# Performance work log

Hardware: AMD Instinct MI355X
Metric: run time of the kernel (lower is better)

Reference implementation:

```python
import jax, jax.numpy as jnp
import numpy as np

N_NODES = 100000
N_EDGES = 3200000
NFEAT = 256
NHID = 256
NOUT = 128


def setup_inputs() -> dict:
    key = jax.random.key(0)
    ks = jax.random.split(key, 8)
    stdv1 = 1.0 / np.sqrt(NHID)
    stdv2 = 1.0 / np.sqrt(NOUT)
    return {
        "feat": jax.random.normal(ks[0], (N_NODES, NFEAT), dtype=jnp.float32),
        "row": jax.random.randint(ks[1], (N_EDGES,), 0, N_NODES, dtype=jnp.int32),
        "col": jax.random.randint(ks[2], (N_EDGES,), 0, N_NODES, dtype=jnp.int32),
        "edge_weight": jax.random.uniform(ks[3], (N_EDGES,), dtype=jnp.float32),
        "W1": jax.random.uniform(ks[4], (NFEAT, NHID), jnp.float32, -stdv1, stdv1),
        "b1": jax.random.uniform(ks[5], (NHID,), jnp.float32, -stdv1, stdv1),
        "W2": jax.random.uniform(ks[6], (NHID, NOUT), jnp.float32, -stdv2, stdv2),
        "b2": jax.random.uniform(ks[7], (NOUT,), jnp.float32, -stdv2, stdv2),
    }


def _spmm(row, col, edge_weight, x, n_nodes):
    # sparse.mm(adj, x): out[i] = sum_e w[e] * x[col[e]] for row[e] == i
    msgs = x[col] * edge_weight[:, None]  # [E, F] gather + scale
    return jax.ops.segment_sum(msgs, row, num_segments=n_nodes)


def reference(feat, row, col, edge_weight, W1, b1, W2, b2):
    # Layer 1: GraphConvolution + ReLU (dropout is identity in eval mode)
    h = _spmm(row, col, edge_weight, feat @ W1, feat.shape[0]) + b1
    h = jax.nn.relu(h)
    # Layer 2: GraphConvolution (no activation on final layer)
    out = _spmm(row, col, edge_weight, h @ W2, feat.shape[0]) + b2
    return out
```

## Files before the change

kernel.cpp:

```cpp
#include <hip/hip_runtime.h>
#include <hip/hip_bf16.h>

#define M_NODES 100000
#define E_EDGES 3200000
#define NBUCK 196
#define BSHIFT 9
#define BCAP 24576
#define K3_EPB 8192
#define K3_BLOCKS 391
#define TILESM 391

typedef __attribute__((ext_vector_type(8))) short short8;
typedef __attribute__((ext_vector_type(4))) float f32x4;
typedef __attribute__((ext_vector_type(2))) float f32x2;

__device__ inline unsigned short f2bf(float f) {
  __hip_bfloat16 h = __float2bfloat16(f);
  return __builtin_bit_cast(unsigned short, h);
}

#if __has_builtin(__builtin_amdgcn_cvt_pk_f32_fp8) && __has_builtin(__builtin_amdgcn_cvt_pk_fp8_f32)
#define HW_FP8 1
#endif

#ifndef HW_FP8
__device__ inline float fp8_dec1(unsigned int b) {
  const unsigned int s = (b >> 7) & 1u, e = (b >> 3) & 15u, m = b & 7u;
  float v;
  if (e == 0) v = (float)m * 0.001953125f;
  else v = __uint_as_float(((e + 120u) << 23) | (m << 20));
  return s ? -v : v;
}
__device__ inline unsigned int fp8_enc1(float x) {
  const unsigned int sb = (__float_as_uint(x) >> 31) << 7;
  float ax = fminf(fabsf(x), 448.f);
  if (ax < 0.0009765625f) return sb;
  const unsigned int xb = __float_as_uint(ax);
  const int ef = (int)(xb >> 23) - 127;
  if (ef < -6) {
    unsigned int m = (unsigned int)(ax * 512.f + 0.5f);
    if (m > 7u) return sb | 0x08u;
    return sb | m;
  }
  unsigned int m3 = ((xb & 0x7FFFFFu) + 0x80000u) >> 20;
  unsigned int e4 = (unsigned int)(ef + 7);
  if (m3 == 8u) { m3 = 0u; e4 += 1u; }
  if (e4 >= 16u) { e4 = 15u; m3 = 6u; }
  return sb | (e4 << 3) | m3;
}
#endif

__device__ inline void fp8x4_dec(unsigned int v, float* o) {
#ifdef HW_FP8
  const f32x2 lo = __builtin_amdgcn_cvt_pk_f32_fp8((int)v, false);
  const f32x2 hi = __builtin_amdgcn_cvt_pk_f32_fp8((int)v, true);
  o[0] = lo[0]; o[1] = lo[1]; o[2] = hi[0]; o[3] = hi[1];
#else
  o[0] = fp8_dec1(v & 255u); o[1] = fp8_dec1((v >> 8) & 255u);
  o[2] = fp8_dec1((v >> 16) & 255u); o[3] = fp8_dec1(v >> 24);
#endif
}
__device__ inline unsigned short fp8x2_enc(float a, float b) {
#ifdef HW_FP8
  const int p = __builtin_amdgcn_cvt_pk_fp8_f32(a, b, 0, false);
  return (unsigned short)(p & 0xFFFF);
#else
  return (unsigned short)(fp8_enc1(a) | (fp8_enc1(b) << 8));
#endif
}

__device__ inline unsigned int epk_col(unsigned int p) { return p >> 15; }
__device__ inline float epk_w(unsigned int p) {
  return __uint_as_float((p & 0x7FFFu) << 16);
}

__device__ inline void pack_one(const float* __restrict__ W,
                                unsigned short* __restrict__ Bf,
                                int idx, int N) {
  const int lane = idx & 63;
  const int f = idx >> 6;
  const int ntile = f % (N >> 4);
  const int kstep = f / (N >> 4);
  const int k0 = (kstep << 5) + ((lane >> 4) << 3);
  const int n = (ntile << 4) + (lane & 15);
  ushort4 lo, hi;
  lo.x = f2bf(W[(size_t)(k0 + 0) * N + n]);
  lo.y = f2bf(W[(size_t)(k0 + 1) * N + n]);
  lo.z = f2bf(W[(size_t)(k0 + 2) * N + n]);
  lo.w = f2bf(W[(size_t)(k0 + 3) * N + n]);
  hi.x = f2bf(W[(size_t)(k0 + 4) * N + n]);
  hi.y = f2bf(W[(size_t)(k0 + 5) * N + n]);
  hi.z = f2bf(W[(size_t)(k0 + 6) * N + n]);
  hi.w = f2bf(W[(size_t)(k0 + 7) * N + n]);
  *(ushort4*)&Bf[(size_t)idx * 8] = lo;
  *(ushort4*)&Bf[(size_t)idx * 8 + 4] = hi;
}

__global__ __launch_bounds__(256) void pack_w_both(
    const float* __restrict__ W1, const float* __restrict__ W2,
    unsigned short* __restrict__ W1f, unsigned short* __restrict__ W2f,
    int* __restrict__ bcnt)
{
  if (blockIdx.x < 32) {
    pack_one(W1, W1f, blockIdx.x * 256 + threadIdx.x, 256);
  } else if (blockIdx.x < 48) {
    pack_one(W2, W2f, (blockIdx.x - 32) * 256 + threadIdx.x, 128);
  } else {
    if (threadIdx.x < NBUCK) bcnt[threadIdx.x] = 0;
  }
}

template<bool A_BF16, bool SWZ>
__global__ __launch_bounds__(256) void gemm_mfma(
    const void* __restrict__ A_, const unsigned short* __restrict__ Bf,
    unsigned char* __restrict__ C, int M, int K, int N, int nTilesN)
{
  __shared__ float cbuf[4][16][132];
  const int wv = threadIdx.x >> 6, lane = threadIdx.x & 63;
  int bm, bn;
  if (SWZ) {
    const int xcd = blockIdx.x & 7;
    const int j = blockIdx.x >> 3;
    bm = xcd * 49 + (j >> 1);
    bn = j & 1;
    if (bm >= TILESM) return;
  } else {
    bm = blockIdx.x / nTilesN;
    bn = blockIdx.x % nTilesN;
  }
  const int m0 = (bm << 8) + (wv << 6);
  const int n0 = bn << 7;
  const int rif = lane & 15, kg = lane >> 4;
  const int nf16 = N >> 4;

  f32x4 acc[4][8] = {};

  const int nK = K >> 5;
  for (int ks = 0; ks < nK; ++ks) {
    const int k0 = (ks << 5) + (kg << 3);
    short8 bfr[8];
    const size_t fbase = ((size_t)ks * nf16 + (n0 >> 4)) * 64 + lane;
#pragma unroll
    for (int nf = 0; nf < 8; ++nf)
      bfr[nf] = *(const short8*)&Bf[(fbase + (size_t)nf * 64) * 8];

    short8 afr[4];
#pragma unroll
    for (int mi = 0; mi < 4; ++mi) {
      const int row = m0 + (mi << 4) + rif;
      if (row < M) {
        if (A_BF16) {
          afr[mi] = *(const short8*)&((const unsigned short*)A_)[(size_t)row * K + k0];
        } else {
          const float* ap = &((const float*)A_)[(size_t)row * K + k0];
          const float4 lo = *(const float4*)ap;
          const float4 hi = *(const float4*)(ap + 4);
          short8 t;
          t[0] = (short)f2bf(lo.x); t[1] = (short)f2bf(lo.y);
          t[2] = (short)f2bf(lo.z); t[3] = (short)f2bf(lo.w);
          t[4] = (short)f2bf(hi.x); t[5] = (short)f2bf(hi.y);
          t[6] = (short)f2bf(hi.z); t[7] = (short)f2bf(hi.w);
          afr[mi] = t;
        }
      } else {
        afr[mi] = (short8)0;
      }
    }
#pragma unroll
    for (int mi = 0; mi < 4; ++mi)
#pragma unroll
      for (int nf = 0; nf < 8; ++nf)
        acc[mi][nf] = __builtin_amdgcn_mfma_f32_16x16x32_bf16(
            afr[mi], bfr[nf], acc[mi][nf], 0, 0, 0);
  }

#pragma unroll
  for (int mi = 0; mi < 4; ++mi) {
#pragma unroll
    for (int nf = 0; nf < 8; ++nf) {
#pragma unroll
      for (int r = 0; r < 4; ++r)
        cbuf[wv][(kg << 2) + r][(nf << 4) + rif] = acc[mi][nf][r];
    }
    __syncthreads();
#pragma unroll
    for (int r = 0; r < 16; ++r) {
      const int row = m0 + (mi << 4) + r;
      if (row < M) {
        const float2 v = *(const float2*)&cbuf[wv][r][lane << 1];
        *(unsigned short*)&C[(size_t)row * N + n0 + (lane << 1)] =
            fp8x2_enc(v.x, v.y);
      }
    }
    __syncthreads();
  }
}

__global__ __launch_bounds__(512) void partition_edges(
    const int* __restrict__ row, const int* __restrict__ col,
    const float* __restrict__ w, int* __restrict__ bcnt,
    int2* __restrict__ P)
{
  __shared__ int2 stage[K3_EPB];
  __shared__ unsigned char sb[K3_EPB];
  __shared__ int hist[NBUCK], cur[NBUCK], delta[NBUCK];
  __shared__ int buf[256];
  const int t = threadIdx.x;
  const int e0 = blockIdx.x * K3_EPB;
  const int e1 = min(e0 + K3_EPB, E_EDGES);
  if (t < NBUCK) hist[t] = 0;
  __syncthreads();
  for (int i = e0 + t; i < e1; i += 512)
    atomicAdd(&hist[row[i] >> BSHIFT], 1);
  __syncthreads();
  int v = 0;
  if (t < 256) {
    v = (t < NBUCK) ? hist[t] : 0;
    buf[t] = v;
  }
  __syncthreads();
  for (int d = 1; d < 256; d <<= 1) {
    int x = 0;
    if (t < 256 && t >= d) x = buf[t - d];
    __syncthreads();
    if (t < 256) buf[t] += x;
    __syncthreads();
  }
  if (t < NBUCK) {
    const int excl = buf[t] - hist[t];
    cur[t] = excl;
    const int g = atomicAdd(&bcnt[t], hist[t]);
    delta[t] = (t * BCAP + g) - excl;
  }
  __syncthreads();
  for (int i = e0 + t; i < e1; i += 512) {
    const int r = row[i];
    const int b = r >> BSHIFT;
    const int pos = atomicAdd(&cur[b], 1);
    stage[pos] = make_int2(col[i] | ((r & 511) << 20), __float_as_int(w[i]));
    sb[pos] = (unsigned char)b;
  }
  __syncthreads();
  const int n = e1 - e0;
  for (int i = t; i < n; i += 512)
    P[delta[sb[i]] + i] = stage[i];
}

__global__ __launch_bounds__(512) void bucket_csr(
    const int* __restrict__ bcnt, const int2* __restrict__ P,
    int* __restrict__ offs, unsigned int* __restrict__ epk)
{
  __shared__ int buf[256];
  __shared__ int rhist[512], rcur[512];
  __shared__ int wsum[8];
  const int t = threadIdx.x;
  const int b = blockIdx.x;
  if (t < 256) buf[t] = (t < NBUCK) ? bcnt[t] : 0;
  __syncthreads();
  for (int d = 1; d < 256; d <<= 1) {
    int x = 0;
    if (t < 256 && t >= d) x = buf[t - d];
    __syncthreads();
    if (t < 256) buf[t] += x;
    __syncthreads();
  }
  const int cnt = bcnt[b];
  const int dst0 = buf[b] - cnt;
  const int src0 = b * BCAP;
  const int row0 = b << BSHIFT;
  if (b == 0 && t == 0) offs[M_NODES] = E_EDGES;
  __syncthreads();
  rhist[t] = 0;
  __syncthreads();
  for (int i = t; i < cnt; i += 512)
    atomicAdd(&rhist[(P[src0 + i].x >> 20) & 511], 1);
  __syncthreads();
  const int lane = t & 63, wv = t >> 6;
  const int v = rhist[t];
  int inc = v;
#pragma unroll
  for (int d = 1; d < 64; d <<= 1) {
    const int x = __shfl_up(inc, d);
    if (lane >= d) inc += x;
  }
  if (lane == 63) wsum[wv] = inc;
  __syncthreads();
  if (t < 8) {
    int sv = wsum[t];
#pragma unroll
    for (int d = 1; d < 8; d <<= 1) {
      const int x = __shfl_up(sv, d);
      if ((int)t >= d) sv += x;
    }
    wsum[t] = sv;
  }
  __syncthreads();
  const int excl = (wv ? wsum[wv - 1] : 0) + inc - v;
  const int gofs = dst0 + excl;
  if (row0 + t < M_NODES) offs[row0 + t] = gofs;
  rcur[t] = gofs;
  __syncthreads();
  for (int i = t; i < cnt; i += 512) {
    const int2 p = P[src0 + i];
    const int rl = (p.x >> 20) & 511;
    const int pos = atomicAdd(&rcur[rl], 1);
    const unsigned int wb = (unsigned int)f2bf(__int_as_float(p.y));
    epk[pos] = (((unsigned int)p.x & 0xFFFFFu) << 15) | wb;
  }
}

__global__ __launch_bounds__(256) void spmm1_fused(
    const int* __restrict__ offs, const unsigned int* __restrict__ epk,
    const unsigned char* __restrict__ X, const float* __restrict__ b1,
    unsigned short* __restrict__ Hb)
{
  const int w = threadIdx.x >> 6, lane = threadIdx.x & 63;
  const int half = lane >> 5, l5 = lane & 31;
  const int r = (blockIdx.x << 2) + w;
  const int s = offs[r], e = offs[r + 1];
  float a[8] = {};
  int i = s;
  for (; i + 8 <= e; i += 8) {
    unsigned int pe[4];
#pragma unroll
    for (int u = 0; u < 4; ++u) pe[u] = epk[i + (u << 1) + half];
    uint2 xv[4];
#pragma unroll
    for (int u = 0; u < 4; ++u)
      xv[u] = *(const uint2*)&X[((size_t)epk_col(pe[u]) << 8) + (l5 << 3)];
#pragma unroll
    for (int u = 0; u < 4; ++u) {
      const float wv = epk_w(pe[u]);
      float f[4], g[4];
      fp8x4_dec(xv[u].x, f);
      fp8x4_dec(xv[u].y, g);
      a[0] = fmaf(wv, f[0], a[0]); a[1] = fmaf(wv, f[1], a[1]);
      a[2] = fmaf(wv, f[2], a[2]); a[3] = fmaf(wv, f[3], a[3]);
      a[4] = fmaf(wv, g[0], a[4]); a[5] = fmaf(wv, g[1], a[5]);
      a[6] = fmaf(wv, g[2], a[6]); a[7] = fmaf(wv, g[3], a[7]);
    }
  }
  for (; i < e; i += 2) {
    const int idx = i + half;
    const unsigned int pe = (idx < e) ? epk[idx] : 0u;
    const float wv = (idx < e) ? epk_w(pe) : 0.f;
    const uint2 xw = *(const uint2*)&X[((size_t)epk_col(pe) << 8) + (l5 << 3)];
    float f[4], g[4];
    fp8x4_dec(xw.x, f);
    fp8x4_dec(xw.y, g);
    a[0] = fmaf(wv, f[0], a[0]); a[1] = fmaf(wv, f[1], a[1]);
    a[2] = fmaf(wv, f[2], a[2]); a[3] = fmaf(wv, f[3], a[3]);
    a[4] = fmaf(wv, g[0], a[4]); a[5] = fmaf(wv, g[1], a[5]);
    a[6] = fmaf(wv, g[2], a[6]); a[7] = fmaf(wv, g[3], a[7]);
  }
#pragma unroll
  for (int j = 0; j < 8; ++j) a[j] += __shfl_xor(a[j], 32);
  if (half == 0) {
    const float4 bv0 = *(const float4*)&b1[l5 << 3];
    const float4 bv1 = *(const float4*)&b1[(l5 << 3) + 4];
    short8 o;
    o[0] = (short)f2bf(fmaxf(a[0] + bv0.x, 0.f));
    o[1] = (short)f2bf(fmaxf(a[1] + bv0.y, 0.f));
    o[2] = (short)f2bf(fmaxf(a[2] + bv0.z, 0.f));
    o[3] = (short)f2bf(fmaxf(a[3] + bv0.w, 0.f));
    o[4] = (short)f2bf(fmaxf(a[4] + bv1.x, 0.f));
    o[5] = (short)f2bf(fmaxf(a[5] + bv1.y, 0.f));
    o[6] = (short)f2bf(fmaxf(a[6] + bv1.z, 0.f));
    o[7] = (short)f2bf(fmaxf(a[7] + bv1.w, 0.f));
    *(short8*)&Hb[((size_t)r << 8) + (l5 << 3)] = o;
  }
}

__global__ __launch_bounds__(256) void spmm2_quad(
    const int* __restrict__ offs, const unsigned int* __restrict__ epk,
    const unsigned char* __restrict__ X, const float* __restrict__ b2,
    float* __restrict__ Y)
{
  const int w = threadIdx.x >> 6, lane = threadIdx.x & 63;
  const int q = lane >> 4, l4 = lane & 15;
  const int r = (blockIdx.x << 2) + w;
  const int s = offs[r], e = offs[r + 1];
  float a[8] = {};
  int i = s;
  for (; i + 16 <= e; i += 16) {
    unsigned int pe[4];
#pragma unroll
    for (int u = 0; u < 4; ++u) pe[u] = epk[i + (u << 2) + q];
    uint2 xv[4];
#pragma unroll
    for (int u = 0; u < 4; ++u)
      xv[u] = *(const uint2*)&X[((size_t)epk_col(pe[u]) << 7) + (l4 << 3)];
#pragma unroll
    for (int u = 0; u < 4; ++u) {
      const float wv = epk_w(pe[u]);
      float f[4], g[4];
      fp8x4_dec(xv[u].x, f);
      fp8x4_dec(xv[u].y, g);
      a[0] = fmaf(wv, f[0], a[0]); a[1] = fmaf(wv, f[1], a[1]);
      a[2] = fmaf(wv, f[2], a[2]); a[3] = fmaf(wv, f[3], a[3]);
      a[4] = fmaf(wv, g[0], a[4]); a[5] = fmaf(wv, g[1], a[5]);
      a[6] = fmaf(wv, g[2], a[6]); a[7] = fmaf(wv, g[3], a[7]);
    }
  }
  for (; i < e; i += 4) {
    const int idx = i + q;
    const unsigned int pe = (idx < e) ? epk[idx] : 0u;
    const float wv = (idx < e) ? epk_w(pe) : 0.f;
    const uint2 xw = *(const uint2*)&X[((size_t)epk_col(pe) << 7) + (l4 << 3)];
    float f[4], g[4];
    fp8x4_dec(xw.x, f);
    fp8x4_dec(xw.y, g);
    a[0] = fmaf(wv, f[0], a[0]); a[1] = fmaf(wv, f[1], a[1]);
    a[2] = fmaf(wv, f[2], a[2]); a[3] = fmaf(wv, f[3], a[3]);
    a[4] = fmaf(wv, g[0], a[4]); a[5] = fmaf(wv, g[1], a[5]);
    a[6] = fmaf(wv, g[2], a[6]); a[7] = fmaf(wv, g[3], a[7]);
  }
#pragma unroll
  for (int j = 0; j < 8; ++j) {
    a[j] += __shfl_xor(a[j], 16);
    a[j] += __shfl_xor(a[j], 32);
  }
  if (q == 0) {
    const float4 bv0 = *(const float4*)&b2[l4 << 3];
    const float4 bv1 = *(const float4*)&b2[(l4 << 3) + 4];
    float* yp = &Y[((size_t)r << 7) + (l4 << 3)];
    *(float4*)yp = make_float4(a[0] + bv0.x, a[1] + bv0.y,
                               a[2] + bv0.z, a[3] + bv0.w);
    *(float4*)(yp + 4) = make_float4(a[4] + bv1.x, a[5] + bv1.y,
                                     a[6] + bv1.z, a[7] + bv1.w);
  }
}

extern "C" void kernel_launch(void* const* d_in, const int* in_sizes, int n_in,
                              void* d_out, int out_size, void* d_ws, size_t ws_size,
                              hipStream_t stream) {
  const float* feat = (const float*)d_in[0];
  const int*   row  = (const int*)d_in[1];
  const int*   col  = (const int*)d_in[2];
  const float* ew   = (const float*)d_in[3];
  const float* W1   = (const float*)d_in[4];
  const float* b1   = (const float*)d_in[5];
  const float* W2   = (const float*)d_in[6];
  const float* b2   = (const float*)d_in[7];
  float* out = (float*)d_out;

  unsigned short* Hb = (unsigned short*)d_ws;
  int2* P = (int2*)d_ws;
  unsigned char* X1 = (unsigned char*)(Hb + (size_t)M_NODES * 256);
  unsigned char* X2 = X1;
  unsigned int* epk = (unsigned int*)(X1 + (size_t)M_NODES * 256);
  int* offs  = (int*)(epk + E_EDGES);
  int* bcnt  = offs + 100004;
  unsigned short* W1f = (unsigned short*)(bcnt + 200);
  unsigned short* W2f = W1f + 65536;

  hipLaunchKernelGGL(pack_w_both, dim3(49), dim3(256), 0, stream,
                     W1, W2, W1f, W2f, bcnt);
  hipLaunchKernelGGL(partition_edges, dim3(K3_BLOCKS), dim3(512), 0, stream,
                     row, col, ew, bcnt, P);
  hipLaunchKernelGGL(bucket_csr, dim3(NBUCK), dim3(512), 0, stream,
                     bcnt, P, offs, epk);

  hipLaunchKernelGGL((gemm_mfma<false, true>), dim3(784), dim3(256), 0,
                     stream, (const void*)feat, W1f, X1, M_NODES, 256, 256, 2);
  hipLaunchKernelGGL(spmm1_fused, dim3(M_NODES / 4), dim3(256), 0, stream,
                     offs, epk, X1, b1, Hb);

  hipLaunchKernelGGL((gemm_mfma<true, false>), dim3(TILESM), dim3(256), 0,
                     stream, (const void*)Hb, W2f, X2, M_NODES, 256, 128, 1);
  hipLaunchKernelGGL(spmm2_quad, dim3(M_NODES / 4), dim3(256), 0, stream,
                     offs, epk, X2, b2, out);
}
```

Before: 332.3 us.

## Fuse weight packing into edge partition and overlap CSR build with GEMM1

Weight packing now runs as extra blocks of the edge-partition kernel, and the bucket-to-CSR pass shares one launch with the first GEMM. The GEMM blocks in that launch use 512 threads so each block covers both 128-column halves, and the bucket counter is zeroed with a memset. GEMM2 becomes a specialised kernel with constant sizes. The aim is fewer launches and letting the small CSR pass overlap the independent GEMM1 work. In exchange, the fused GEMM drops the XCD block swizzle and needs a larger shared buffer, which may reduce occupancy.

```diff
diff --git a/kernel.cpp b/kernel.cpp
--- a/kernel.cpp
+++ b/kernel.cpp
@@ -96,116 +96,26 @@
   *(ushort4*)&Bf[(size_t)idx * 8 + 4] = hi;
 }
 
-__global__ __launch_bounds__(256) void pack_w_both(
-    const float* __restrict__ W1, const float* __restrict__ W2,
-    unsigned short* __restrict__ W1f, unsigned short* __restrict__ W2f,
-    int* __restrict__ bcnt)
-{
-  if (blockIdx.x < 32) {
-    pack_one(W1, W1f, blockIdx.x * 256 + threadIdx.x, 256);
-  } else if (blockIdx.x < 48) {
-    pack_one(W2, W2f, (blockIdx.x - 32) * 256 + threadIdx.x, 128);
-  } else {
-    if (threadIdx.x < NBUCK) bcnt[threadIdx.x] = 0;
-  }
-}
-
-template<bool A_BF16, bool SWZ>
-__global__ __launch_bounds__(256) void gemm_mfma(
-    const void* __restrict__ A_, const unsigned short* __restrict__ Bf,
-    unsigned char* __restrict__ C, int M, int K, int N, int nTilesN)
-{
-  __shared__ float cbuf[4][16][132];
-  const int wv = threadIdx.x >> 6, lane = threadIdx.x & 63;
-  int bm, bn;
-  if (SWZ) {
-    const int xcd = blockIdx.x & 7;
-    const int j = blockIdx.x >> 3;
-    bm = xcd * 49 + (j >> 1);
-    bn = j & 1;
-    if (bm >= TILESM) return;
-  } else {
-    bm = blockIdx.x / nTilesN;
-    bn = blockIdx.x % nTilesN;
-  }
-  const int m0 = (bm << 8) + (wv << 6);
-  const int n0 = bn << 7;
-  const int rif = lane & 15, kg = lane >> 4;
-  const int nf16 = N >> 4;
-
-  f32x4 acc[4][8] = {};
-
-  const int nK = K >> 5;
-  for (int ks = 0; ks < nK; ++ks) {
-    const int k0 = (ks << 5) + (kg << 3);
-    short8 bfr[8];
-    const size_t fbase = ((size_t)ks * nf16 + (n0 >> 4)) * 64 + lane;
-#pragma unroll
-    for (int nf = 0; nf < 8; ++nf)
-      bfr[nf] = *(const short8*)&Bf[(fbase + (size_t)nf * 64) * 8];
-
-    short8 afr[4];
-#pragma unroll
-    for (int mi = 0; mi < 4; ++mi) {
-      const int row = m0 + (mi << 4) + rif;
-      if (row < M) {
-        if (A_BF16) {
-          afr[mi] = *(const short8*)&((const unsigned short*)A_)[(size_t)row * K + k0];
-        } else {
-          const float* ap = &((const float*)A_)[(size_t)row * K + k0];
-          const float4 lo = *(const float4*)ap;
-          const float4 hi = *(const float4*)(ap + 4);
-          short8 t;
-          t[0] = (short)f2bf(lo.x); t[1] = (short)f2bf(lo.y);
-          t[2] = (short)f2bf(lo.z); t[3] = (short)f2bf(lo.w);
-          t[4] = (short)f2bf(hi.x); t[5] = (short)f2bf(hi.y);
-          t[6] = (short)f2bf(hi.z); t[7] = (short)f2bf(hi.w);
-          afr[mi] = t;
-        }
-      } else {
-        afr[mi] = (short8)0;
-      }
-    }
-#pragma unroll
-    for (int mi = 0; mi < 4; ++mi)
-#pragma unroll
-      for (int nf = 0; nf < 8; ++nf)
-        acc[mi][nf] = __builtin_amdgcn_mfma_f32_16x16x32_bf16(
-            afr[mi], bfr[nf], acc[mi][nf], 0, 0, 0);
-  }
-
-#pragma unroll
-  for (int mi = 0; mi < 4; ++mi) {
-#pragma unroll
-    for (int nf = 0; nf < 8; ++nf) {
-#pragma unroll
-      for (int r = 0; r < 4; ++r)
-        cbuf[wv][(kg << 2) + r][(nf << 4) + rif] = acc[mi][nf][r];
-    }
-    __syncthreads();
-#pragma unroll
-    for (int r = 0; r < 16; ++r) {
-      const int row = m0 + (mi << 4) + r;
-      if (row < M) {
-        const float2 v = *(const float2*)&cbuf[wv][r][lane << 1];
-        *(unsigned short*)&C[(size_t)row * N + n0 + (lane << 1)] =
-            fp8x2_enc(v.x, v.y);
-      }
-    }
-    __syncthreads();
-  }
-}
-
-__global__ __launch_bounds__(512) void partition_edges(
+__global__ __launch_bounds__(512) void prep_fused(
     const int* __restrict__ row, const int* __restrict__ col,
     const float* __restrict__ w, int* __restrict__ bcnt,
-    int2* __restrict__ P)
+    int2* __restrict__ P,
+    const float* __restrict__ W1, const float* __restrict__ W2,
+    unsigned short* __restrict__ W1f, unsigned short* __restrict__ W2f)
 {
   __shared__ int2 stage[K3_EPB];
   __shared__ unsigned char sb[K3_EPB];
   __shared__ int hist[NBUCK], cur[NBUCK], delta[NBUCK];
   __shared__ int buf[256];
   const int t = threadIdx.x;
+
+  if (blockIdx.x >= K3_BLOCKS) {
+    const int pb = blockIdx.x - K3_BLOCKS;
+    if (pb < 16) pack_one(W1, W1f, pb * 512 + t, 256);
+    else         pack_one(W2, W2f, (pb - 16) * 512 + t, 128);
+    return;
+  }
+
   const int e0 = blockIdx.x * K3_EPB;
   const int e1 = min(e0 + K3_EPB, E_EDGES);
   if (t < NBUCK) hist[t] = 0;
@@ -246,66 +156,197 @@
     P[delta[sb[i]] + i] = stage[i];
 }
 
-__global__ __launch_bounds__(512) void bucket_csr(
+__global__ __launch_bounds__(512) void csr_gemm1_fused(
     const int* __restrict__ bcnt, const int2* __restrict__ P,
-    int* __restrict__ offs, unsigned int* __restrict__ epk)
+    int* __restrict__ offs, unsigned int* __restrict__ epk,
+    const float* __restrict__ A_, const unsigned short* __restrict__ Bf,
+    unsigned char* __restrict__ C)
 {
-  __shared__ int buf[256];
-  __shared__ int rhist[512], rcur[512];
-  __shared__ int wsum[8];
+  __shared__ __align__(16) char smem[8 * 16 * 132 * 4];
   const int t = threadIdx.x;
-  const int b = blockIdx.x;
-  if (t < 256) buf[t] = (t < NBUCK) ? bcnt[t] : 0;
-  __syncthreads();
-  for (int d = 1; d < 256; d <<= 1) {
-    int x = 0;
-    if (t < 256 && t >= d) x = buf[t - d];
-    __syncthreads();
-    if (t < 256) buf[t] += x;
-    __syncthreads();
-  }
-  const int cnt = bcnt[b];
-  const int dst0 = buf[b] - cnt;
-  const int src0 = b * BCAP;
-  const int row0 = b << BSHIFT;
-  if (b == 0 && t == 0) offs[M_NODES] = E_EDGES;
-  __syncthreads();
-  rhist[t] = 0;
-  __syncthreads();
-  for (int i = t; i < cnt; i += 512)
-    atomicAdd(&rhist[(P[src0 + i].x >> 20) & 511], 1);
-  __syncthreads();
-  const int lane = t & 63, wv = t >> 6;
-  const int v = rhist[t];
-  int inc = v;
-#pragma unroll
-  for (int d = 1; d < 64; d <<= 1) {
-    const int x = __shfl_up(inc, d);
-    if (lane >= d) inc += x;
-  }
-  if (lane == 63) wsum[wv] = inc;
-  __syncthreads();
-  if (t < 8) {
-    int sv = wsum[t];
-#pragma unroll
-    for (int d = 1; d < 8; d <<= 1) {
-      const int x = __shfl_up(sv, d);
-      if ((int)t >= d) sv += x;
-    }
-    wsum[t] = sv;
-  }
-  __syncthreads();
-  const int excl = (wv ? wsum[wv - 1] : 0) + inc - v;
-  const int gofs = dst0 + excl;
-  if (row0 + t < M_NODES) offs[row0 + t] = gofs;
-  rcur[t] = gofs;
-  __syncthreads();
-  for (int i = t; i < cnt; i += 512) {
-    const int2 p = P[src0 + i];
-    const int rl = (p.x >> 20) & 511;
-    const int pos = atomicAdd(&rcur[rl], 1);
-    const unsigned int wb = (unsigned int)f2bf(__int_as_float(p.y));
-    epk[pos] = (((unsigned int)p.x & 0xFFFFFu) << 15) | wb;
+
+  if (blockIdx.x < NBUCK) {
+    int* buf   = (int*)smem;
+    int* rhist = buf + 256;
+    int* rcur  = rhist + 512;
+    int* wsum  = rcur + 512;
+    const int b = blockIdx.x;
+    if (t < 256) buf[t] = (t < NBUCK) ? bcnt[t] : 0;
+    __syncthreads();
+    for (int d = 1; d < 256; d <<= 1) {
+      int x = 0;
+      if (t < 256 && t >= d) x = buf[t - d];
+      __syncthreads();
+      if (t < 256) buf[t] += x;
+      __syncthreads();
+    }
+    const int cnt = bcnt[b];
+    const int dst0 = buf[b] - cnt;
+    const int src0 = b * BCAP;
+    const int row0 = b << BSHIFT;
+    if (b == 0 && t == 0) offs[M_NODES] = E_EDGES;
+    __syncthreads();
+    rhist[t] = 0;
+    __syncthreads();
+    for (int i = t; i < cnt; i += 512)
+      atomicAdd(&rhist[(P[src0 + i].x >> 20) & 511], 1);
+    __syncthreads();
+    const int lane = t & 63, wv = t >> 6;
+    const int v = rhist[t];
+    int inc = v;
+#pragma unroll
+    for (int d = 1; d < 64; d <<= 1) {
+      const int x = __shfl_up(inc, d);
+      if (lane >= d) inc += x;
+    }
+    if (lane == 63) wsum[wv] = inc;
+    __syncthreads();
+    if (t < 8) {
+      int sv = wsum[t];
+#pragma unroll
+      for (int d = 1; d < 8; d <<= 1) {
+        const int x = __shfl_up(sv, d);
+        if ((int)t >= d) sv += x;
+      }
+      wsum[t] = sv;
+    }
+    __syncthreads();
+    const int excl = (wv ? wsum[wv - 1] : 0) + inc - v;
+    const int gofs = dst0 + excl;
+    if (row0 + t < M_NODES) offs[row0 + t] = gofs;
+    rcur[t] = gofs;
+    __syncthreads();
+    for (int i = t; i < cnt; i += 512) {
+      const int2 p = P[src0 + i];
+      const int rl = (p.x >> 20) & 511;
+      const int pos = atomicAdd(&rcur[rl], 1);
+      const unsigned int wb = (unsigned int)f2bf(__int_as_float(p.y));
+      epk[pos] = (((unsigned int)p.x & 0xFFFFFu) << 15) | wb;
+    }
+    return;
+  }
+
+  float (*cbuf)[16][132] = reinterpret_cast<float (*)[16][132]>(smem);
+  const int bm = blockIdx.x - NBUCK;
+  const int wv = t >> 6, lane = t & 63;
+  const int m0 = (bm << 8) + ((wv & 3) << 6);
+  const int n0 = (wv >> 2) << 7;
+  const int rif = lane & 15, kg = lane >> 4;
+
+  f32x4 acc[4][8] = {};
+
+#pragma unroll
+  for (int ks = 0; ks < 8; ++ks) {
+    const int k0 = (ks << 5) + (kg << 3);
+    short8 bfr[8];
+    const size_t fbase = ((size_t)(ks << 4) + (n0 >> 4)) * 64 + lane;
+#pragma unroll
+    for (int nf = 0; nf < 8; ++nf)
+      bfr[nf] = *(const short8*)&Bf[(fbase + (size_t)nf * 64) * 8];
+
+    short8 afr[4];
+#pragma unroll
+    for (int mi = 0; mi < 4; ++mi) {
+      const int row = m0 + (mi << 4) + rif;
+      if (row < M_NODES) {
+        const float* ap = &A_[(size_t)row * 256 + k0];
+        const float4 lo = *(const float4*)ap;
+        const float4 hi = *(const float4*)(ap + 4);
+        short8 tt;
+        tt[0] = (short)f2bf(lo.x); tt[1] = (short)f2bf(lo.y);
+        tt[2] = (short)f2bf(lo.z); tt[3] = (short)f2bf(lo.w);
+        tt[4] = (short)f2bf(hi.x); tt[5] = (short)f2bf(hi.y);
+        tt[6] = (short)f2bf(hi.z); tt[7] = (short)f2bf(hi.w);
+        afr[mi] = tt;
+      } else {
+        afr[mi] = (short8)0;
+      }
+    }
+#pragma unroll
+    for (int mi = 0; mi < 4; ++mi)
+#pragma unroll
+      for (int nf = 0; nf < 8; ++nf)
+        acc[mi][nf] = __builtin_amdgcn_mfma_f32_16x16x32_bf16(
+            afr[mi], bfr[nf], acc[mi][nf], 0, 0, 0);
+  }
+
+#pragma unroll
+  for (int mi = 0; mi < 4; ++mi) {
+#pragma unroll
+    for (int nf = 0; nf < 8; ++nf) {
+#pragma unroll
+      for (int r = 0; r < 4; ++r)
+        cbuf[wv][(kg << 2) + r][(nf << 4) + rif] = acc[mi][nf][r];
+    }
+    __syncthreads();
+#pragma unroll
+    for (int r = 0; r < 16; ++r) {
+      const int row = m0 + (mi << 4) + r;
+      if (row < M_NODES) {
+        const float2 v = *(const float2*)&cbuf[wv][r][lane << 1];
+        *(unsigned short*)&C[(size_t)row * 256 + n0 + (lane << 1)] =
+            fp8x2_enc(v.x, v.y);
+      }
+    }
+    __syncthreads();
+  }
+}
+
+__global__ __launch_bounds__(256) void gemm2_mfma(
+    const unsigned short* __restrict__ A_, const unsigned short* __restrict__ Bf,
+    unsigned char* __restrict__ C)
+{
+  __shared__ float cbuf[4][16][132];
+  const int wv = threadIdx.x >> 6, lane = threadIdx.x & 63;
+  const int m0 = (blockIdx.x << 8) + (wv << 6);
+  const int rif = lane & 15, kg = lane >> 4;
+
+  f32x4 acc[4][8] = {};
+
+#pragma unroll
+  for (int ks = 0; ks < 8; ++ks) {
+    const int k0 = (ks << 5) + (kg << 3);
+    short8 bfr[8];
+    const size_t fbase = ((size_t)(ks << 3)) * 64 + lane;
+#pragma unroll
+    for (int nf = 0; nf < 8; ++nf)
+      bfr[nf] = *(const short8*)&Bf[(fbase + (size_t)nf * 64) * 8];
+
+    short8 afr[4];
+#pragma unroll
+    for (int mi = 0; mi < 4; ++mi) {
+      const int row = m0 + (mi << 4) + rif;
+      afr[mi] = (row < M_NODES)
+          ? *(const short8*)&A_[(size_t)row * 256 + k0]
+          : (short8)0;
+    }
+#pragma unroll
+    for (int mi = 0; mi < 4; ++mi)
+#pragma unroll
+      for (int nf = 0; nf < 8; ++nf)
+        acc[mi][nf] = __builtin_amdgcn_mfma_f32_16x16x32_bf16(
+            afr[mi], bfr[nf], acc[mi][nf], 0, 0, 0);
+  }
+
+#pragma unroll
+  for (int mi = 0; mi < 4; ++mi) {
+#pragma unroll
+    for (int nf = 0; nf < 8; ++nf) {
+#pragma unroll
+      for (int r = 0; r < 4; ++r)
+        cbuf[wv][(kg << 2) + r][(nf << 4) + rif] = acc[mi][nf][r];
+    }
+    __syncthreads();
+#pragma unroll
+    for (int r = 0; r < 16; ++r) {
+      const int row = m0 + (mi << 4) + r;
+      if (row < M_NODES) {
+        const float2 v = *(const float2*)&cbuf[wv][r][lane << 1];
+        *(unsigned short*)&C[(size_t)row * 128 + (lane << 1)] =
+            fp8x2_enc(v.x, v.y);
+      }
+    }
+    __syncthreads();
   }
 }
 
@@ -454,20 +495,15 @@
   unsigned short* W1f = (unsigned short*)(bcnt + 200);
   unsigned short* W2f = W1f + 65536;
 
-  hipLaunchKernelGGL(pack_w_both, dim3(49), dim3(256), 0, stream,
-                     W1, W2, W1f, W2f, bcnt);
-  hipLaunchKernelGGL(partition_edges, dim3(K3_BLOCKS), dim3(512), 0, stream,
-                     row, col, ew, bcnt, P);
-  hipLaunchKernelGGL(bucket_csr, dim3(NBUCK), dim3(512), 0, stream,
-                     bcnt, P, offs, epk);
-
-  hipLaunchKernelGGL((gemm_mfma<false, true>), dim3(784), dim3(256), 0,
-                     stream, (const void*)feat, W1f, X1, M_NODES, 256, 256, 2);
+  hipMemsetAsync(bcnt, 0, NBUCK * sizeof(int), stream);
+  hipLaunchKernelGGL(prep_fused, dim3(K3_BLOCKS + 24), dim3(512), 0, stream,
+                     row, col, ew, bcnt, P, W1, W2, W1f, W2f);
+  hipLaunchKernelGGL(csr_gemm1_fused, dim3(NBUCK + TILESM), dim3(512), 0,
+                     stream, bcnt, P, offs, epk, feat, W1f, X1);
   hipLaunchKernelGGL(spmm1_fused, dim3(M_NODES / 4), dim3(256), 0, stream,
                      offs, epk, X1, b1, Hb);
-
-  hipLaunchKernelGGL((gemm_mfma<true, false>), dim3(TILESM), dim3(256), 0,
-                     stream, (const void*)Hb, W2f, X2, M_NODES, 256, 128, 1);
+  hipLaunchKernelGGL(gemm2_mfma, dim3(TILESM), dim3(256), 0, stream,
+                     (const unsigned short*)Hb, W2f, X2);
   hipLaunchKernelGGL(spmm2_quad, dim3(M_NODES / 4), dim3(256), 0, stream,
                      offs, epk, X2, b2, out);
 }
```

New measurement: 337.2 us. No clear change (+1.5%).
